# Kernel tuning notes

Measured on AMD Instinct MI355X. Metric: run time of the kernel, lower is better.

The kernel has to match this reference:

```python
import jax, jax.numpy as jnp
import numpy as np


def setup_inputs() -> dict:
    key = jax.random.key(0)
    ks = jax.random.split(key, 5)
    B, D, U = 16384, 512, 512
    return {
        "inputs": jax.random.normal(ks[0], (B, D), dtype=jnp.float32),
        "h_prev": jax.random.normal(ks[1], (B, U), dtype=jnp.float32),
        "update_kernel": jax.random.normal(ks[2], (D + U, U), dtype=jnp.float32) * 0.03,
        "reset_kernel": jax.random.normal(ks[3], (D + U, U), dtype=jnp.float32) * 0.03,
        "hidden_kernel": jax.random.normal(ks[4], (D + U, U), dtype=jnp.float32) * 0.03,
        "update_bias": jnp.zeros((U,), dtype=jnp.float32),
        "reset_bias": jnp.zeros((U,), dtype=jnp.float32),
        "hidden_bias": jnp.zeros((U,), dtype=jnp.float32),
    }


def reference(inputs, h_prev, update_kernel, reset_kernel, hidden_kernel,
              update_bias, reset_bias, hidden_bias):
    # fused_input: [B, D+U]
    fused = jnp.concatenate([inputs, h_prev], axis=-1)
    zg = jax.nn.sigmoid(fused @ update_kernel + update_bias)   # update gate [B,U]
    rg = jax.nn.sigmoid(fused @ reset_kernel + reset_bias)     # reset gate  [B,U]
    h_tilde = jnp.tanh(
        jnp.concatenate([inputs, rg * h_prev], axis=-1) @ hidden_kernel + hidden_bias
    )
    ht = (1.0 - zg) * h_prev + zg * h_tilde
    return ht
```

## Files before the change

### kernel.cpp

```cpp
#include <hip/hip_runtime.h>
#include <hip/hip_bf16.h>
#include <math.h>

typedef __attribute__((ext_vector_type(4))) float f32x4;
typedef __attribute__((ext_vector_type(8))) float f32x8;
typedef __bf16 bf16x8 __attribute__((ext_vector_type(8)));
typedef unsigned short u16;
typedef u16 u16x8 __attribute__((ext_vector_type(8)));
typedef void __attribute__((address_space(1))) * as1p;
typedef void __attribute__((address_space(3))) * as3p;

__device__ __forceinline__ unsigned short f2bf(float f) {
    union { float f; unsigned int u; } v; v.f = f;
    unsigned int u = v.u;
    u += 0x7fffu + ((u >> 16) & 1u);
    return (unsigned short)(u >> 16);
}

__device__ __forceinline__ float bf2f(unsigned short b) {
    union { unsigned int u; float f; } v;
    v.u = ((unsigned int)b) << 16;
    return v.f;
}

__device__ __forceinline__ float fast_tanh(float v) {
    float vc = fminf(fmaxf(v, -15.f), 15.f);
    float e = __expf(2.f * vc);
    return (e - 1.f) / (e + 1.f);
}

__global__ void cvt_xh(const float* __restrict__ x, const float* __restrict__ h,
                       u16* __restrict__ xb, u16* __restrict__ hb, int n4) {
    int i = blockIdx.x * blockDim.x + threadIdx.x;
    int stride = gridDim.x * blockDim.x;
    const float4* x4 = (const float4*)x;
    const float4* h4 = (const float4*)h;
    ushort4* xb4 = (ushort4*)xb;
    ushort4* hb4 = (ushort4*)hb;
    for (; i < n4; i += stride) {
        float4 v = x4[i];
        xb4[i] = make_ushort4(f2bf(v.x), f2bf(v.y), f2bf(v.z), f2bf(v.w));
        float4 w = h4[i];
        hb4[i] = make_ushort4(f2bf(w.x), f2bf(w.y), f2bf(w.z), f2bf(w.w));
    }
}

__global__ void tr_cvt3(const float* __restrict__ s0, const float* __restrict__ s1,
                        const float* __restrict__ s2, u16* __restrict__ d0,
                        u16* __restrict__ d1, u16* __restrict__ d2) {
    __shared__ float t[32][33];
    const float* src = (blockIdx.z == 0) ? s0 : (blockIdx.z == 1) ? s1 : s2;
    u16* dst = (blockIdx.z == 0) ? d0 : (blockIdx.z == 1) ? d1 : d2;
    int n0 = blockIdx.x * 32;
    int k0 = blockIdx.y * 32;
    int tx = threadIdx.x, ty = threadIdx.y;
#pragma unroll
    for (int i = 0; i < 4; ++i)
        t[ty + i * 8][tx] = src[(size_t)(k0 + ty + i * 8) * 512 + n0 + tx];
    __syncthreads();
#pragma unroll
    for (int i = 0; i < 4; ++i)
        dst[(size_t)(n0 + ty + i * 8) * 1024 + k0 + tx] = f2bf(t[tx][ty + i * 8]);
}

__device__ __forceinline__ void stage_sw(const u16* g, int gstride, u16* lds, int tid) {
#pragma unroll
    for (int i = 0; i < 4; ++i) {
        int ob = i * 4096 + ((tid >> 6) << 10);
        int o = ob + ((tid & 63) << 4);
        int row = o >> 7;
        int cb = (o & 127) ^ ((row & 7) << 4);
        const u16* gp = g + (size_t)row * gstride + (cb >> 1);
        __builtin_amdgcn_global_load_lds((as1p)(void*)gp, (as3p)(void*)(lds + (ob >> 1)), 16, 0, 0);
    }
}

__device__ __forceinline__ bf16x8 ld_frag(const u16* region, int r, int kb) {
    int byte = (r << 7) + (kb ^ ((r & 7) << 4));
    return *(const bf16x8*)((const char*)region + byte);
}

__device__ __forceinline__ void compute_tile(const u16* LA, const u16* LB,
                                             int wr, int wc, int l, f32x4 (&acc)[4][4]) {
    int fr = l & 15;
    int kbb = (l >> 4) << 4;
#pragma unroll
    for (int q = 0; q < 2; ++q) {
        bf16x8 a[4], b[4];
#pragma unroll
        for (int m = 0; m < 4; ++m)
            a[m] = ld_frag(LA, wr * 64 + m * 16 + fr, q * 64 + kbb);
#pragma unroll
        for (int n = 0; n < 4; ++n)
            b[n] = ld_frag(LB, wc * 64 + n * 16 + fr, q * 64 + kbb);
#pragma unroll
        for (int m = 0; m < 4; ++m)
#pragma unroll
            for (int n = 0; n < 4; ++n)
                acc[m][n] = __builtin_amdgcn_mfma_f32_16x16x32_bf16(a[m], b[n], acc[m][n], 0, 0, 0);
    }
}

template<typename AF, typename BF>
__device__ __forceinline__ void kloop(AF ga, BF gb, u16* lds, int tid,
                                      int wr, int wc, int l, f32x4 (&acc)[4][4]) {
    stage_sw(ga(0), 512, lds, tid);
    stage_sw(gb(0), 1024, lds + 8192, tid);
    __syncthreads();
#pragma unroll
    for (int i = 0; i < 15; ++i) {
        u16* nxt = lds + ((i + 1) & 1) * 16384;
        const u16* cur = lds + (i & 1) * 16384;
        stage_sw(ga(i + 1), 512, nxt, tid);
        stage_sw(gb(i + 1), 1024, nxt + 8192, tid);
        compute_tile(cur, cur + 8192, wr, wc, l, acc);
        __syncthreads();
    }
    compute_tile(lds + 16384, lds + 16384 + 8192, wr, wc, l, acc);
}

__device__ __forceinline__ void scatter_acc(float* tf, const f32x4 (&acc)[4][4],
                                            int wr, int wc, int l) {
    int colb = wc * 64;
    int rowb = wr * 64 + ((l >> 4) << 2);
#pragma unroll
    for (int n = 0; n < 4; ++n) {
        int col = colb + n * 16 + (l & 15);
#pragma unroll
        for (int m = 0; m < 4; ++m) {
            int row0 = rowb + m * 16;
#pragma unroll
            for (int r = 0; r < 4; ++r)
                tf[(row0 + r) * 128 + col] = acc[m][n][r];
        }
    }
}

__global__ __launch_bounds__(256) void gr_k(
    const u16* __restrict__ Xb, const u16* __restrict__ Hb, const u16* __restrict__ Wt,
    const float* __restrict__ rb_, u16* __restrict__ rgh) {
    __shared__ u16 lds[2 * 16384];
    int tid = threadIdx.x;
    int l = tid & 63, w = tid >> 6;
    int wr = w >> 1, wc = w & 1;
    int swz = (blockIdx.x & 7) * 64 + (blockIdx.x >> 3);
    int mb = swz >> 2, nb = swz & 3;
    int m0 = mb * 128, n0 = nb * 128;
    f32x4 acc[4][4];
#pragma unroll
    for (int m = 0; m < 4; ++m)
#pragma unroll
        for (int n = 0; n < 4; ++n) acc[m][n] = (f32x4){0.f, 0.f, 0.f, 0.f};

    auto ga = [&](int t) -> const u16* {
        return (t < 8) ? (Xb + (size_t)m0 * 512 + t * 64)
                       : (Hb + (size_t)m0 * 512 + (t - 8) * 64);
    };
    auto gb = [&](int t) -> const u16* { return Wt + (size_t)n0 * 1024 + t * 64; };
    kloop(ga, gb, lds, tid, wr, wc, l, acc);

    __syncthreads();
    float* tf = (float*)lds;
    scatter_acc(tf, acc, wr, wc, l);
    __syncthreads();
#pragma unroll
    for (int i = 0; i < 8; ++i) {
        int chunk = i * 256 + tid;
        int row = chunk >> 4;
        int c8 = (chunk & 15) << 3;
        const float* src = &tf[row * 128 + c8];
        int gcol = n0 + c8;
        size_t gbase = (size_t)(m0 + row) * 512 + gcol;
        u16x8 h8 = *(const u16x8*)&Hb[gbase];
        u16x8 o;
#pragma unroll
        for (int j = 0; j < 8; ++j) {
            float v = src[j] + rb_[gcol + j];
            float s = 1.f / (1.f + __expf(-v));
            o[j] = f2bf(s * bf2f(h8[j]));
        }
        *(u16x8*)&rgh[gbase] = o;
    }
}

__device__ __forceinline__ void stage32(const u16* g, int gstride, u16* region, int tid) {
#pragma unroll
    for (int i = 0; i < 2; ++i) {
        int ob = i * 4096 + ((tid >> 6) << 10);
        int o = ob + ((tid & 63) << 4);
        int row = o >> 6;
        int cb = (o & 63) ^ ((row & 3) << 4);
        const u16* gp = g + (size_t)row * gstride + (cb >> 1);
        __builtin_amdgcn_global_load_lds((as1p)(void*)gp, (as3p)(void*)(region + (ob >> 1)), 16, 0, 0);
    }
}

__device__ __forceinline__ bf16x8 ld32(const u16* region, int r, int kb) {
    int byte = (r << 6) + (kb ^ ((r & 3) << 4));
    return *(const bf16x8*)((const char*)region + byte);
}

__global__ __launch_bounds__(256, 2) void ghz_k(
    const u16* __restrict__ Xb, const u16* __restrict__ Hb, const u16* __restrict__ rgh,
    const u16* __restrict__ Wht, const u16* __restrict__ Wzt,
    const float* __restrict__ ub, const float* __restrict__ hb,
    float* __restrict__ out) {
    __shared__ u16 lds[2 * 16384];
    int tid = threadIdx.x;
    int l = tid & 63, w = tid >> 6;
    int wr = w >> 1, wc = w & 1;
    int swz = (blockIdx.x & 7) * 64 + (blockIdx.x >> 3);
    int mb = swz >> 2, nb = swz & 3;
    int m0 = mb * 128, n0 = nb * 128;

    f32x4 acc_h[4][4], acc_z[4][4];
#pragma unroll
    for (int m = 0; m < 4; ++m)
#pragma unroll
        for (int n = 0; n < 4; ++n) {
            acc_h[m][n] = (f32x4){0.f, 0.f, 0.f, 0.f};
            acc_z[m][n] = (f32x4){0.f, 0.f, 0.f, 0.f};
        }

    auto ah = [&](int t) -> const u16* {
        return (t < 16) ? (Xb + (size_t)m0 * 512 + t * 32)
                        : (rgh + (size_t)m0 * 512 + (t - 16) * 32);
    };
    auto az = [&](int t) -> const u16* {
        return Hb + (size_t)m0 * 512 + (t - 16) * 32;
    };
    auto bhp = [&](int t) -> const u16* { return Wht + (size_t)n0 * 1024 + t * 32; };
    auto bzp = [&](int t) -> const u16* { return Wzt + (size_t)n0 * 1024 + t * 32; };

    const int fr = l & 15;
    const int kbb = (l >> 4) << 4;

    stage32(ah(0), 512, lds, tid);
    stage32(bhp(0), 1024, lds + 8192, tid);
    stage32(bzp(0), 1024, lds + 12288, tid);
    __syncthreads();

#pragma unroll
    for (int i = 0; i < 32; ++i) {
        const u16* cur = lds + (i & 1) * 16384;
        if (i < 31) {
            u16* nxt = lds + ((i + 1) & 1) * 16384;
            stage32(ah(i + 1), 512, nxt, tid);
            if (i + 1 >= 16) stage32(az(i + 1), 512, nxt + 4096, tid);
            stage32(bhp(i + 1), 1024, nxt + 8192, tid);
            stage32(bzp(i + 1), 1024, nxt + 12288, tid);
        }
        const u16* Ahr = cur;
        const u16* Azr = (i < 16) ? cur : (cur + 4096);
        const u16* Bhr = cur + 8192;
        const u16* Bzr = cur + 12288;
        bf16x8 a[4], azf[4], bh4[4], bz4[4];
#pragma unroll
        for (int m = 0; m < 4; ++m) {
            a[m]   = ld32(Ahr, wr * 64 + m * 16 + fr, kbb);
            azf[m] = ld32(Azr, wr * 64 + m * 16 + fr, kbb);
        }
#pragma unroll
        for (int n = 0; n < 4; ++n) {
            bh4[n] = ld32(Bhr, wc * 64 + n * 16 + fr, kbb);
            bz4[n] = ld32(Bzr, wc * 64 + n * 16 + fr, kbb);
        }
#pragma unroll
        for (int m = 0; m < 4; ++m)
#pragma unroll
            for (int n = 0; n < 4; ++n) {
                acc_h[m][n] = __builtin_amdgcn_mfma_f32_16x16x32_bf16(a[m], bh4[n], acc_h[m][n], 0, 0, 0);
                acc_z[m][n] = __builtin_amdgcn_mfma_f32_16x16x32_bf16(azf[m], bz4[n], acc_z[m][n], 0, 0, 0);
            }
        __syncthreads();
    }

    float* tf = (float*)lds;
    scatter_acc(tf, acc_z, wr, wc, l);
    __syncthreads();
    u16x8 zreg[8];
#pragma unroll
    for (int i = 0; i < 8; ++i) {
        int chunk = i * 256 + tid;
        int row = chunk >> 4;
        int c8 = (chunk & 15) << 3;
        f32x8 vz = *(const f32x8*)&tf[row * 128 + c8];
        f32x8 ubv = *(const f32x8*)&ub[n0 + c8];
#pragma unroll
        for (int j = 0; j < 8; ++j) {
            float s = 1.f / (1.f + __expf(-(vz[j] + ubv[j])));
            zreg[i][j] = f2bf(s);
        }
    }
    __syncthreads();
    scatter_acc(tf, acc_h, wr, wc, l);
    __syncthreads();
#pragma unroll
    for (int i = 0; i < 8; ++i) {
        int chunk = i * 256 + tid;
        int row = chunk >> 4;
        int c8 = (chunk & 15) << 3;
        int gcol = n0 + c8;
        size_t gbase = (size_t)(m0 + row) * 512 + gcol;
        f32x8 vh = *(const f32x8*)&tf[row * 128 + c8];
        f32x8 hbv = *(const f32x8*)&hb[gcol];
        u16x8 h8 = *(const u16x8*)&Hb[gbase];
        f32x8 o;
#pragma unroll
        for (int j = 0; j < 8; ++j) {
            float t = fast_tanh(vh[j] + hbv[j]);
            float h0 = bf2f(h8[j]);
            float z = bf2f(zreg[i][j]);
            o[j] = h0 + z * (t - h0);
        }
        *(f32x8*)&out[gbase] = o;
    }
}

extern "C" void kernel_launch(void* const* d_in, const int* in_sizes, int n_in,
                              void* d_out, int out_size, void* d_ws, size_t ws_size,
                              hipStream_t stream) {
    const float* x  = (const float*)d_in[0];
    const float* h  = (const float*)d_in[1];
    const float* wz = (const float*)d_in[2];
    const float* wr = (const float*)d_in[3];
    const float* wh = (const float*)d_in[4];
    const float* ub = (const float*)d_in[5];
    const float* rb = (const float*)d_in[6];
    const float* hb = (const float*)d_in[7];
    float* out = (float*)d_out;

    const int B = 16384;
    char* ws = (char*)d_ws;
    size_t off = 0;
    u16* Xb  = (u16*)(ws + off); off += (size_t)B * 512 * 2;
    u16* Hb  = (u16*)(ws + off); off += (size_t)B * 512 * 2;
    u16* Wzt = (u16*)(ws + off); off += (size_t)512 * 1024 * 2;
    u16* Wrt = (u16*)(ws + off); off += (size_t)512 * 1024 * 2;
    u16* Wht = (u16*)(ws + off); off += (size_t)512 * 1024 * 2;
    u16* rgh = (u16*)(ws + off); off += (size_t)B * 512 * 2;

    cvt_xh<<<2048, 256, 0, stream>>>(x, h, Xb, Hb, B * 512 / 4);

    dim3 tb(32, 8), tg(16, 32, 3);
    tr_cvt3<<<tg, tb, 0, stream>>>(wz, wr, wh, Wzt, Wrt, Wht);

    gr_k<<<512, 256, 0, stream>>>(Xb, Hb, Wrt, rb, rgh);
    ghz_k<<<512, 256, 0, stream>>>(Xb, Hb, rgh, Wht, Wzt, ub, hb, out);
}
```

Baseline: 98.58 us.

## Fuse fp32-to-bf16 activation conversion into the reset-gate GEMM kernel

Drops the separate cvt_xh pass. The reset-gate GEMM now loads fp32 x and h_prev directly, converts them to bf16 in registers and writes them swizzled into LDS. Blocks with nb==0 also write the bf16 copies to global memory for the later kernel. The epilogue reads fp32 h_prev instead of the bf16 copy. This saves a kernel launch and one full read/write pass over the activations, but the A-operand staging now goes through registers instead of async global-to-LDS loads, which could reduce latency hiding in the main loop.

```diff
diff --git a/kernel.cpp b/kernel.cpp
--- a/kernel.cpp
+++ b/kernel.cpp
@@ -29,31 +29,19 @@
     return (e - 1.f) / (e + 1.f);
 }
 
-__global__ void cvt_xh(const float* __restrict__ x, const float* __restrict__ h,
-                       u16* __restrict__ xb, u16* __restrict__ hb, int n4) {
-    int i = blockIdx.x * blockDim.x + threadIdx.x;
-    int stride = gridDim.x * blockDim.x;
-    const float4* x4 = (const float4*)x;
-    const float4* h4 = (const float4*)h;
-    ushort4* xb4 = (ushort4*)xb;
-    ushort4* hb4 = (ushort4*)hb;
-    for (; i < n4; i += stride) {
-        float4 v = x4[i];
-        xb4[i] = make_ushort4(f2bf(v.x), f2bf(v.y), f2bf(v.z), f2bf(v.w));
-        float4 w = h4[i];
-        hb4[i] = make_ushort4(f2bf(w.x), f2bf(w.y), f2bf(w.z), f2bf(w.w));
-    }
-}
-
-__global__ void tr_cvt3(const float* __restrict__ s0, const float* __restrict__ s1,
+__global__ void prepw_k(const float* __restrict__ s0, const float* __restrict__ s1,
                         const float* __restrict__ s2, u16* __restrict__ d0,
                         u16* __restrict__ d1, u16* __restrict__ d2) {
     __shared__ float t[32][33];
-    const float* src = (blockIdx.z == 0) ? s0 : (blockIdx.z == 1) ? s1 : s2;
-    u16* dst = (blockIdx.z == 0) ? d0 : (blockIdx.z == 1) ? d1 : d2;
-    int n0 = blockIdx.x * 32;
-    int k0 = blockIdx.y * 32;
-    int tx = threadIdx.x, ty = threadIdx.y;
+    int b = blockIdx.x;
+    int z = b >> 9;
+    int rem = b & 511;
+    const float* src = (z == 0) ? s0 : (z == 1) ? s1 : s2;
+    u16* dst = (z == 0) ? d0 : (z == 1) ? d1 : d2;
+    int n0 = (rem & 15) * 32;
+    int k0 = (rem >> 4) * 32;
+    int tid = threadIdx.x;
+    int tx = tid & 31, ty = tid >> 5;
 #pragma unroll
     for (int i = 0; i < 4; ++i)
         t[ty + i * 8][tx] = src[(size_t)(k0 + ty + i * 8) * 512 + n0 + tx];
@@ -101,24 +89,6 @@
     }
 }
 
-template<typename AF, typename BF>
-__device__ __forceinline__ void kloop(AF ga, BF gb, u16* lds, int tid,
-                                      int wr, int wc, int l, f32x4 (&acc)[4][4]) {
-    stage_sw(ga(0), 512, lds, tid);
-    stage_sw(gb(0), 1024, lds + 8192, tid);
-    __syncthreads();
-#pragma unroll
-    for (int i = 0; i < 15; ++i) {
-        u16* nxt = lds + ((i + 1) & 1) * 16384;
-        const u16* cur = lds + (i & 1) * 16384;
-        stage_sw(ga(i + 1), 512, nxt, tid);
-        stage_sw(gb(i + 1), 1024, nxt + 8192, tid);
-        compute_tile(cur, cur + 8192, wr, wc, l, acc);
-        __syncthreads();
-    }
-    compute_tile(lds + 16384, lds + 16384 + 8192, wr, wc, l, acc);
-}
-
 __device__ __forceinline__ void scatter_acc(float* tf, const f32x4 (&acc)[4][4],
                                             int wr, int wc, int l) {
     int colb = wc * 64;
@@ -137,8 +107,9 @@
 }
 
 __global__ __launch_bounds__(256) void gr_k(
-    const u16* __restrict__ Xb, const u16* __restrict__ Hb, const u16* __restrict__ Wt,
-    const float* __restrict__ rb_, u16* __restrict__ rgh) {
+    const float* __restrict__ x, const float* __restrict__ hprev,
+    const u16* __restrict__ Wt, const float* __restrict__ rb_,
+    u16* __restrict__ rgh, u16* __restrict__ Xb, u16* __restrict__ Hb) {
     __shared__ u16 lds[2 * 16384];
     int tid = threadIdx.x;
     int l = tid & 63, w = tid >> 6;
@@ -146,18 +117,61 @@
     int swz = (blockIdx.x & 7) * 64 + (blockIdx.x >> 3);
     int mb = swz >> 2, nb = swz & 3;
     int m0 = mb * 128, n0 = nb * 128;
+    bool writeAB = (nb == 0);
     f32x4 acc[4][4];
 #pragma unroll
     for (int m = 0; m < 4; ++m)
 #pragma unroll
         for (int n = 0; n < 4; ++n) acc[m][n] = (f32x4){0.f, 0.f, 0.f, 0.f};
 
-    auto ga = [&](int t) -> const u16* {
-        return (t < 8) ? (Xb + (size_t)m0 * 512 + t * 64)
-                       : (Hb + (size_t)m0 * 512 + (t - 8) * 64);
-    };
-    auto gb = [&](int t) -> const u16* { return Wt + (size_t)n0 * 1024 + t * 64; };
-    kloop(ga, gb, lds, tid, wr, wc, l, acc);
+    const int ar = tid >> 1;
+    const int ahc = tid & 1;
+
+    auto asrc = [&](int t) -> const float* {
+        return (t < 8) ? &x[(size_t)(m0 + ar) * 512 + t * 64 + ahc * 32]
+                       : &hprev[(size_t)(m0 + ar) * 512 + (t - 8) * 64 + ahc * 32];
+    };
+    auto adst = [&](int t) -> u16* {
+        return (t < 8) ? &Xb[(size_t)(m0 + ar) * 512 + t * 64 + ahc * 32]
+                       : &Hb[(size_t)(m0 + ar) * 512 + (t - 8) * 64 + ahc * 32];
+    };
+    auto writeA = [&](int t, u16* Abuf, const float4* av) {
+#pragma unroll
+        for (int j = 0; j < 4; ++j) {
+            u16x8 v;
+            v[0] = f2bf(av[2 * j].x); v[1] = f2bf(av[2 * j].y);
+            v[2] = f2bf(av[2 * j].z); v[3] = f2bf(av[2 * j].w);
+            v[4] = f2bf(av[2 * j + 1].x); v[5] = f2bf(av[2 * j + 1].y);
+            v[6] = f2bf(av[2 * j + 1].z); v[7] = f2bf(av[2 * j + 1].w);
+            int byte = (ar << 7) + (((ahc * 64) + j * 16) ^ ((ar & 7) << 4));
+            *(u16x8*)((char*)Abuf + byte) = v;
+            if (writeAB) *(u16x8*)(adst(t) + j * 8) = v;
+        }
+    };
+
+    {
+        float4 av[8];
+        const float* s = asrc(0);
+#pragma unroll
+        for (int j = 0; j < 8; ++j) av[j] = *(const float4*)(s + j * 4);
+        stage_sw(Wt + (size_t)n0 * 1024, 1024, lds + 8192, tid);
+        writeA(0, lds, av);
+    }
+    __syncthreads();
+
+    for (int i = 0; i < 15; ++i) {
+        u16* nxt = lds + ((i + 1) & 1) * 16384;
+        const u16* cur = lds + (i & 1) * 16384;
+        float4 av[8];
+        const float* s = asrc(i + 1);
+#pragma unroll
+        for (int j = 0; j < 8; ++j) av[j] = *(const float4*)(s + j * 4);
+        stage_sw(Wt + (size_t)n0 * 1024 + (i + 1) * 64, 1024, nxt + 8192, tid);
+        compute_tile(cur, cur + 8192, wr, wc, l, acc);
+        writeA(i + 1, nxt, av);
+        __syncthreads();
+    }
+    compute_tile(lds + 16384, lds + 16384 + 8192, wr, wc, l, acc);
 
     __syncthreads();
     float* tf = (float*)lds;
@@ -171,13 +185,13 @@
         const float* src = &tf[row * 128 + c8];
         int gcol = n0 + c8;
         size_t gbase = (size_t)(m0 + row) * 512 + gcol;
-        u16x8 h8 = *(const u16x8*)&Hb[gbase];
+        f32x8 h8 = *(const f32x8*)&hprev[gbase];
+        f32x8 bv = *(const f32x8*)&rb_[gcol];
         u16x8 o;
 #pragma unroll
         for (int j = 0; j < 8; ++j) {
-            float v = src[j] + rb_[gcol + j];
-            float s = 1.f / (1.f + __expf(-v));
-            o[j] = f2bf(s * bf2f(h8[j]));
+            float s_ = 1.f / (1.f + __expf(-(src[j] + bv[j])));
+            o[j] = f2bf(s_ * h8[j]);
         }
         *(u16x8*)&rgh[gbase] = o;
     }
@@ -340,11 +354,7 @@
     u16* Wht = (u16*)(ws + off); off += (size_t)512 * 1024 * 2;
     u16* rgh = (u16*)(ws + off); off += (size_t)B * 512 * 2;
 
-    cvt_xh<<<2048, 256, 0, stream>>>(x, h, Xb, Hb, B * 512 / 4);
-
-    dim3 tb(32, 8), tg(16, 32, 3);
-    tr_cvt3<<<tg, tb, 0, stream>>>(wz, wr, wh, Wzt, Wrt, Wht);
-
-    gr_k<<<512, 256, 0, stream>>>(Xb, Hb, Wrt, rb, rgh);
+    prepw_k<<<1536, 256, 0, stream>>>(wz, wr, wh, Wzt, Wrt, Wht);
+    gr_k<<<512, 256, 0, stream>>>(x, h, Wrt, rb, rgh, Xb, Hb);
     ghz_k<<<512, 256, 0, stream>>>(Xb, Hb, rgh, Wht, Wzt, ub, hb, out);
 }
```

After: 118.2 us. 19.9% more time.
